# Kernel optimization log

Hardware: AMD Instinct MI355X
Metric: run time of the kernel (lower is better)

Reference implementation:

```python
import jax, jax.numpy as jnp
import numpy as np

N_NODES = 100000
N_EDGES = 3200000
NEG_SLOPE = 0.2  # PyG GATConv default
EPS = 1e-16      # PyG softmax denominator guard


def setup_inputs() -> dict:
    key = jax.random.key(0)
    ks = jax.random.split(key, 12)
    x = jax.random.normal(ks[0], (N_NODES, 4), dtype=jnp.float32)
    edge_index = jax.random.randint(ks[1], (2, N_EDGES), 0, N_NODES, dtype=jnp.int32)
    # conv1: in=4, heads=4, out=16, concat -> 64
    W1 = jax.random.normal(ks[2], (4, 64), dtype=jnp.float32) * 0.5
    a_src1 = jax.random.normal(ks[3], (4, 16), dtype=jnp.float32) * 0.3
    a_dst1 = jax.random.normal(ks[4], (4, 16), dtype=jnp.float32) * 0.3
    b1 = jnp.zeros((64,), dtype=jnp.float32)
    # conv2: in=64, heads=1, out=2, no concat
    W2 = jax.random.normal(ks[5], (64, 2), dtype=jnp.float32) * 0.2
    a_src2 = jax.random.normal(ks[6], (1, 2), dtype=jnp.float32) * 0.3
    a_dst2 = jax.random.normal(ks[7], (1, 2), dtype=jnp.float32) * 0.3
    b2 = jnp.zeros((2,), dtype=jnp.float32)
    return dict(x=x, edge_index=edge_index, W1=W1, a_src1=a_src1, a_dst1=a_dst1,
                b1=b1, W2=W2, a_src2=a_src2, a_dst2=a_dst2, b2=b2)


def _gat_layer(h_in, src, dst, W, a_s, a_d, b, heads, out_dim, concat):
    n = h_in.shape[0]
    h = (h_in @ W).reshape(n, heads, out_dim)            # [N, H, F]
    alpha_s = jnp.einsum('nhf,hf->nh', h, a_s)           # [N, H]
    alpha_d = jnp.einsum('nhf,hf->nh', h, a_d)
    e = jax.nn.leaky_relu(alpha_s[src] + alpha_d[dst], NEG_SLOPE)  # [E, H]
    # segment softmax over incoming edges of each dst node
    m = jax.ops.segment_max(e, dst, num_segments=n)      # [N, H]
    e = jnp.exp(e - m[dst])
    s = jax.ops.segment_sum(e, dst, num_segments=n)
    alpha = e / (s[dst] + EPS)                            # [E, H]
    msg = h[src] * alpha[:, :, None]                      # [E, H, F]
    out = jax.ops.segment_sum(msg, dst, num_segments=n)   # [N, H, F]
    if concat:
        out = out.reshape(n, heads * out_dim)
    else:
        out = out.mean(axis=1)
    return out + b


def reference(x, edge_index, W1, a_src1, a_dst1, b1, W2, a_src2, a_dst2, b2):
    n = x.shape[0]
    loop = jnp.arange(n, dtype=edge_index.dtype)
    src = jnp.concatenate([edge_index[0], loop])  # PyG add_self_loops=True
    dst = jnp.concatenate([edge_index[1], loop])
    h = jax.nn.elu(_gat_layer(x, src, dst, W1, a_src1, a_dst1, b1, 4, 16, True))
    h = _gat_layer(h, src, dst, W2, a_src2, a_dst2, b2, 1, 2, False)
    return jax.nn.log_softmax(h, axis=1)
```

## Files before the change

kernel.cpp:

```cpp
#include <hip/hip_runtime.h>
#include <hip/hip_fp16.h>
#include <math.h>

#define NEG_SLOPE 0.2f
#define EPS_F 1e-16f

#define P1_NB 256
#define P1S_THREADS 1024
#define MAX_BEDGES 10240

__device__ __forceinline__ float leaky(float v) {
    return v >= 0.f ? v : NEG_SLOPE * v;
}

__global__ void k_phaseA(const float* __restrict__ x, const float* __restrict__ W1,
                         const float* __restrict__ a_src1, const float* __restrict__ a_dst1,
                         __half* __restrict__ h1h, float* __restrict__ as1,
                         float* __restrict__ ad1, int N) {
    int node = blockIdx.x * 4 + (threadIdx.x >> 6);
    if (node >= N) return;
    int lane = threadIdx.x & 63;
    float x0 = x[node * 4 + 0], x1 = x[node * 4 + 1];
    float x2 = x[node * 4 + 2], x3 = x[node * 4 + 3];
    float h = x0 * W1[lane] + x1 * W1[64 + lane] + x2 * W1[128 + lane] + x3 * W1[192 + lane];
    h1h[(size_t)node * 64 + lane] = __float2half(h);
    float as = h * a_src1[lane];
    float ad = h * a_dst1[lane];
#pragma unroll
    for (int m = 8; m >= 1; m >>= 1) {
        as += __shfl_xor(as, m, 16);
        ad += __shfl_xor(ad, m, 16);
    }
    if ((lane & 15) == 0) {
        int head = lane >> 4;
        as1[node * 4 + head] = as;
        ad1[node * 4 + head] = ad;
    }
}

__global__ void k_p1hist(const int* __restrict__ dst, int* __restrict__ histT,
                         int E, int chunk, int nbucket) {
    __shared__ int cnt[512];
    int blk = blockIdx.x, t = threadIdx.x;
    for (int i = t; i < nbucket; i += P1S_THREADS) cnt[i] = 0;
    __syncthreads();
    int s = blk * chunk, e = min(E, s + chunk);
    for (int i = s + t; i < e; i += P1S_THREADS)
        atomicAdd(&cnt[dst[i] >> 8], 1);
    __syncthreads();
    for (int i = t; i < nbucket; i += P1S_THREADS)
        histT[i * P1_NB + blk] = cnt[i];
}

__global__ void k_scan1(const int* __restrict__ in, int* __restrict__ out,
                        int* __restrict__ blockSums, int M) {
    __shared__ int sdata[256];
    int t = threadIdx.x;
    int base = blockIdx.x * 2048 + t * 8;
    int v[8];
    int total = 0;
#pragma unroll
    for (int k = 0; k < 8; ++k) {
        int idx = base + k;
        v[k] = (idx < M) ? in[idx] : 0;
        total += v[k];
    }
    sdata[t] = total;
    __syncthreads();
    for (int off = 1; off < 256; off <<= 1) {
        int x = (t >= off) ? sdata[t - off] : 0;
        __syncthreads();
        sdata[t] += x;
        __syncthreads();
    }
    int run = sdata[t] - total;
#pragma unroll
    for (int k = 0; k < 8; ++k) {
        int idx = base + k;
        if (idx < M) out[idx] = run;
        run += v[k];
    }
    if (t == 255) blockSums[blockIdx.x] = sdata[255];
}

__global__ void k_scan23(int* __restrict__ out, const int* __restrict__ blockSums, int M) {
    int t = threadIdx.x;
    int base = blockIdx.x * 2048 + t * 8;
    int off = 0;
    for (int j = 0; j < (int)blockIdx.x; ++j) off += blockSums[j];
#pragma unroll
    for (int k = 0; k < 8; ++k) {
        int idx = base + k;
        if (idx < M) out[idx] += off;
    }
}

__global__ void k_p1scatter(const int* __restrict__ src, const int* __restrict__ dst,
                            const int* __restrict__ baseT, unsigned int* __restrict__ packed,
                            int E, int chunk, int nbucket) {
    __shared__ int cnt[512];
    int blk = blockIdx.x, t = threadIdx.x;
    for (int i = t; i < nbucket; i += P1S_THREADS) cnt[i] = baseT[i * P1_NB + blk];
    __syncthreads();
    int s = blk * chunk, e = min(E, s + chunk);
    for (int i = s + t; i < e; i += P1S_THREADS) {
        int d = dst[i];
        int pos = atomicAdd(&cnt[d >> 8], 1);
        packed[pos] = ((unsigned int)(d & 255) << 23) | (unsigned int)src[i];
    }
}

__global__ void k_fineL1(const unsigned int* __restrict__ packed, const int* __restrict__ baseT,
                         const __half* __restrict__ h1h, const float* __restrict__ as1,
                         const float* __restrict__ ad1, const float* __restrict__ b1,
                         const float* __restrict__ W2, const float* __restrict__ a_src2,
                         const float* __restrict__ a_dst2,
                         int* __restrict__ csr, int* __restrict__ rowptr,
                         float4* __restrict__ node2, int N, int E) {
    __shared__ int cnt[256];
    __shared__ int off[256];
    __shared__ int cur[256];
    __shared__ unsigned int eb[MAX_BEDGES];

    int b = blockIdx.x, t = threadIdx.x;
    int nbucket = gridDim.x;
    int startE = baseT[b * P1_NB];
    int endE = (b == nbucket - 1) ? E : baseT[(b + 1) * P1_NB];
    int ne = endE - startE;
    if (ne > MAX_BEDGES) ne = MAX_BEDGES;

    if (t < 256) cnt[t] = 0;
    __syncthreads();
    for (int i = t; i < ne; i += 1024)
        atomicAdd(&cnt[packed[startE + i] >> 23], 1);
    __syncthreads();
    if (t < 256) cur[t] = cnt[t];
    __syncthreads();
    for (int o = 1; o < 256; o <<= 1) {
        int v = (t < 256 && t >= o) ? cur[t - o] : 0;
        __syncthreads();
        if (t < 256) cur[t] += v;
        __syncthreads();
    }
    if (t < 256) {
        int excl = cur[t] - cnt[t];
        off[t] = excl;
        int node = (b << 8) + t;
        if (node < N) rowptr[node] = startE + excl;
    }
    if (b == 0 && t == 0) rowptr[N] = E;
    __syncthreads();
    if (t < 256) cur[t] = off[t];
    __syncthreads();
    for (int i = t; i < ne; i += 1024) {
        unsigned int p = packed[startE + i];
        int pos = atomicAdd(&cur[p >> 23], 1);
        eb[pos] = p;
    }
    __syncthreads();
    for (int i = t; i < ne; i += 1024)
        csr[startE + i] = (int)(eb[i] & 0x7FFFFFu);

    int wave = t >> 6;
    int lane = t & 63;
    int head4 = lane & 3;
    int j     = lane >> 2;
    int sub   = lane >> 4;
    int fl    = lane & 15;
    int h     = fl >> 2;
    int nodeBase = b << 8;

    for (int q = 0; q < 16; ++q) {
        int local = wave * 16 + q;
        int node = nodeBase + local;
        if (node >= N) break;
        int beg = off[local];
        int end = beg + cnt[local];

        float ad_s1 = ad1[node * 4 + head4];
        float pself4 = __expf(leaky(as1[node * 4 + head4] + ad_s1));
        float psum = (lane < 4) ? pself4 : 0.f;

        float pselfF = __shfl(pself4, h);
        float a0 = 0.f, a1 = 0.f, a2 = 0.f, a3 = 0.f;
        if (sub == 0) {
            float2 raw = *(const float2*)(h1h + ((size_t)node << 6) + (fl << 2));
            __half2 h01 = *reinterpret_cast<__half2*>(&raw.x);
            __half2 h23 = *reinterpret_cast<__half2*>(&raw.y);
            float2 f01 = __half22float2(h01), f23 = __half22float2(h23);
            a0 = pselfF * f01.x; a1 = pselfF * f01.y;
            a2 = pselfF * f23.x; a3 = pselfF * f23.y;
        }

        for (int c = beg; c < end; c += 16) {
            int e = c + j;
            bool valid = e < end;
            int s = (int)(eb[valid ? e : beg] & 0x7FFFFFu);
            float v = leaky(as1[s * 4 + head4] + ad_s1);
            float p = valid ? __expf(v) : 0.f;
            psum += p;

            int s_q[4];
#pragma unroll
            for (int m = 0; m < 4; ++m) s_q[m] = __shfl(s, m * 16 + sub * 4);
            float2 raw[4];
#pragma unroll
            for (int m = 0; m < 4; ++m)
                raw[m] = *(const float2*)(h1h + ((size_t)s_q[m] << 6) + (fl << 2));
            float p_q[4];
#pragma unroll
            for (int m = 0; m < 4; ++m) p_q[m] = __shfl(p, m * 16 + sub * 4 + h);
#pragma unroll
            for (int m = 0; m < 4; ++m) {
                __half2 h01 = *reinterpret_cast<__half2*>(&raw[m].x);
                __half2 h23 = *reinterpret_cast<__half2*>(&raw[m].y);
                float2 f01 = __half22float2(h01), f23 = __half22float2(h23);
                a0 = fmaf(p_q[m], f01.x, a0);
                a1 = fmaf(p_q[m], f01.y, a1);
                a2 = fmaf(p_q[m], f23.x, a2);
                a3 = fmaf(p_q[m], f23.y, a3);
            }
        }

        a0 += __shfl_xor(a0, 16); a0 += __shfl_xor(a0, 32);
        a1 += __shfl_xor(a1, 16); a1 += __shfl_xor(a1, 32);
        a2 += __shfl_xor(a2, 16); a2 += __shfl_xor(a2, 32);
        a3 += __shfl_xor(a3, 16); a3 += __shfl_xor(a3, 32);

#pragma unroll
        for (int m = 4; m <= 32; m <<= 1) psum += __shfl_xor(psum, m);
        float psumF = __shfl(psum, h);
        float inv = 1.f / (psumF + EPS_F);

        float4 b1v = ((const float4*)b1)[fl];
        float o0 = a0 * inv + b1v.x;
        float o1 = a1 * inv + b1v.y;
        float o2 = a2 * inv + b1v.z;
        float o3 = a3 * inv + b1v.w;
        float e0 = o0 > 0.f ? o0 : expm1f(o0);
        float e1 = o1 > 0.f ? o1 : expm1f(o1);
        float e2 = o2 > 0.f ? o2 : expm1f(o2);
        float e3 = o3 > 0.f ? o3 : expm1f(o3);

        float4 w01 = ((const float4*)W2)[fl * 2];
        float4 w23 = ((const float4*)W2)[fl * 2 + 1];
        float c0 = e0 * w01.x + e1 * w01.z + e2 * w23.x + e3 * w23.z;
        float c1 = e0 * w01.y + e1 * w01.w + e2 * w23.y + e3 * w23.w;
#pragma unroll
        for (int m = 8; m >= 1; m >>= 1) {
            c0 += __shfl_xor(c0, m);
            c1 += __shfl_xor(c1, m);
        }
        if (lane == 0) {
            float as2 = c0 * a_src2[0] + c1 * a_src2[1];
            float ad2 = c0 * a_dst2[0] + c1 * a_dst2[1];
            node2[node] = make_float4(c0, c1, as2, ad2);
        }
    }
}

__global__ void k_layer2(const int* __restrict__ rowptr, const int* __restrict__ csr,
                         const float4* __restrict__ node2, const float* __restrict__ b2,
                         float* __restrict__ out, int N) {
    int node = blockIdx.x * 16 + (threadIdx.x >> 4);
    if (node >= N) return;
    int sl = threadIdx.x & 15;

    float4 me = node2[node];
    float ad = me.w;
    int beg = rowptr[node], end = rowptr[node + 1];

    float psum = 0.f, a0 = 0.f, a1 = 0.f;
    for (int e = beg + sl; e < end; e += 16) {
        float4 sn = node2[csr[e]];
        float p = __expf(leaky(sn.z + ad));
        psum += p;
        a0 = fmaf(p, sn.x, a0);
        a1 = fmaf(p, sn.y, a1);
    }
    if (sl == 0) {
        float p = __expf(leaky(me.z + ad));
        psum += p;
        a0 = fmaf(p, me.x, a0);
        a1 = fmaf(p, me.y, a1);
    }
#pragma unroll
    for (int m = 8; m >= 1; m >>= 1) {
        psum += __shfl_xor(psum, m);
        a0 += __shfl_xor(a0, m);
        a1 += __shfl_xor(a1, m);
    }
    if (sl == 0) {
        float inv = 1.f / (psum + EPS_F);
        float o0 = a0 * inv + b2[0];
        float o1 = a1 * inv + b2[1];
        float mx = fmaxf(o0, o1);
        float lse = mx + logf(__expf(o0 - mx) + __expf(o1 - mx));
        out[node * 2 + 0] = o0 - lse;
        out[node * 2 + 1] = o1 - lse;
    }
}


extern "C" void kernel_launch(void* const* d_in, const int* in_sizes, int n_in,
                              void* d_out, int out_size, void* d_ws, size_t ws_size,
                              hipStream_t stream) {
    const float* x      = (const float*)d_in[0];
    const int*   ei     = (const int*)d_in[1];
    const float* W1     = (const float*)d_in[2];
    const float* a_src1 = (const float*)d_in[3];
    const float* a_dst1 = (const float*)d_in[4];
    const float* b1     = (const float*)d_in[5];
    const float* W2     = (const float*)d_in[6];
    const float* a_src2 = (const float*)d_in[7];
    const float* a_dst2 = (const float*)d_in[8];
    const float* b2     = (const float*)d_in[9];
    float* out = (float*)d_out;

    int N = in_sizes[0] / 4;
    int E = in_sizes[1] / 2;
    const int* e_src = ei;
    const int* e_dst = ei + E;

    int nbucket = (N + 255) >> 8;
    int M = nbucket * P1_NB;

    char* w = (char*)d_ws;
    auto alloc = [&](size_t bytes) -> void* {
        void* p = (void*)w;
        w += (bytes + 255) & ~(size_t)255;
        return p;
    };
    __half* h1h       = (__half*)alloc((size_t)N * 64 * 2);
    float*  as1       = (float*)alloc((size_t)N * 4 * 4);
    float*  ad1       = (float*)alloc((size_t)N * 4 * 4);
    float4* node2     = (float4*)alloc((size_t)N * 16);
    int*    rowptr    = (int*)alloc((size_t)(N + 1) * 4);
    int*    histT     = (int*)alloc((size_t)M * 4);
    int*    baseT     = (int*)alloc((size_t)M * 4);
    int*    blockSums = (int*)alloc(256 * 4);
    int*    csr       = (int*)alloc((size_t)E * 4);
    unsigned int* packed = (unsigned int*)alloc((size_t)E * 4);

    int chunk = (E + P1_NB - 1) / P1_NB;
    int nbScan = (M + 2047) / 2048;
    int nodeb = (N + 3) / 4;

    k_phaseA<<<nodeb, 256, 0, stream>>>(x, W1, a_src1, a_dst1, h1h, as1, ad1, N);
    k_p1hist<<<P1_NB, P1S_THREADS, 0, stream>>>(e_dst, histT, E, chunk, nbucket);
    k_scan1<<<nbScan, 256, 0, stream>>>(histT, baseT, blockSums, M);
    k_scan23<<<nbScan, 256, 0, stream>>>(baseT, blockSums, M);
    k_p1scatter<<<P1_NB, P1S_THREADS, 0, stream>>>(e_src, e_dst, baseT, packed, E, chunk, nbucket);
    k_fineL1<<<nbucket, 1024, 0, stream>>>(packed, baseT, h1h, as1, ad1, b1, W2,
                                           a_src2, a_dst2, csr, rowptr, node2, N, E);
    k_layer2<<<(N + 15) / 16, 256, 0, stream>>>(rowptr, csr, node2, b2, out, N);
}
```

Before: 249.7 us.

## Fold scan fixup into consumers, pack layer-2 node data as half, use fast ELU

Removes the k_scan23 launch by having k_p1scatter and k_fineL1 add the per-scan-block prefix computed from blockSums on the fly. Packs the layer-2 per-node record (features and attention logits) into four halves instead of four floats, halving the bytes fetched by the random gathers in k_layer2. Replaces expm1f in the ELU with __expf minus one. The half packing and fast exp lose precision, and the serial prefix loop over blockSums is done by a single thread per block.

```diff
diff --git a/kernel.cpp b/kernel.cpp
--- a/kernel.cpp
+++ b/kernel.cpp
@@ -8,6 +8,7 @@
 #define P1_NB 256
 #define P1S_THREADS 1024
 #define MAX_BEDGES 10240
+#define SCAN_SHIFT 11
 
 __device__ __forceinline__ float leaky(float v) {
     return v >= 0.f ? v : NEG_SLOPE * v;
@@ -83,24 +84,22 @@
     if (t == 255) blockSums[blockIdx.x] = sdata[255];
 }
 
-__global__ void k_scan23(int* __restrict__ out, const int* __restrict__ blockSums, int M) {
-    int t = threadIdx.x;
-    int base = blockIdx.x * 2048 + t * 8;
-    int off = 0;
-    for (int j = 0; j < (int)blockIdx.x; ++j) off += blockSums[j];
-#pragma unroll
-    for (int k = 0; k < 8; ++k) {
-        int idx = base + k;
-        if (idx < M) out[idx] += off;
-    }
-}
-
 __global__ void k_p1scatter(const int* __restrict__ src, const int* __restrict__ dst,
-                            const int* __restrict__ baseT, unsigned int* __restrict__ packed,
+                            const int* __restrict__ baseT, const int* __restrict__ blockSums,
+                            int nbScan, unsigned int* __restrict__ packed,
                             int E, int chunk, int nbucket) {
     __shared__ int cnt[512];
+    __shared__ int pre[64];
     int blk = blockIdx.x, t = threadIdx.x;
-    for (int i = t; i < nbucket; i += P1S_THREADS) cnt[i] = baseT[i * P1_NB + blk];
+    if (t == 0) {
+        int run = 0;
+        for (int j = 0; j < nbScan; ++j) { pre[j] = run; run += blockSums[j]; }
+    }
+    __syncthreads();
+    for (int i = t; i < nbucket; i += P1S_THREADS) {
+        int idx = i * P1_NB + blk;
+        cnt[i] = baseT[idx] + pre[idx >> SCAN_SHIFT];
+    }
     __syncthreads();
     int s = blk * chunk, e = min(E, s + chunk);
     for (int i = s + t; i < e; i += P1S_THREADS) {
@@ -111,26 +110,40 @@
 }
 
 __global__ void k_fineL1(const unsigned int* __restrict__ packed, const int* __restrict__ baseT,
+                         const int* __restrict__ blockSums, int nbScan,
                          const __half* __restrict__ h1h, const float* __restrict__ as1,
                          const float* __restrict__ ad1, const float* __restrict__ b1,
                          const float* __restrict__ W2, const float* __restrict__ a_src2,
                          const float* __restrict__ a_dst2,
                          int* __restrict__ csr, int* __restrict__ rowptr,
-                         float4* __restrict__ node2, int N, int E) {
+                         uint2* __restrict__ node2, int N, int E) {
     __shared__ int cnt[256];
     __shared__ int off[256];
     __shared__ int cur[256];
+    __shared__ int sePre[2];
     __shared__ unsigned int eb[MAX_BEDGES];
 
     int b = blockIdx.x, t = threadIdx.x;
     int nbucket = gridDim.x;
-    int startE = baseT[b * P1_NB];
-    int endE = (b == nbucket - 1) ? E : baseT[(b + 1) * P1_NB];
+    if (t == 0) {
+        int idx0 = b * P1_NB, idx1 = (b + 1) * P1_NB;
+        int sb0 = idx0 >> SCAN_SHIFT, sb1 = idx1 >> SCAN_SHIFT;
+        int run = 0, p0 = 0, p1 = 0;
+        for (int j = 0; j < nbScan; ++j) {
+            if (j == sb0) p0 = run;
+            if (j == sb1) p1 = run;
+            run += blockSums[j];
+        }
+        sePre[0] = p0; sePre[1] = p1;
+    }
+    if (t < 256) cnt[t] = 0;
+    __syncthreads();
+    int startE = baseT[b * P1_NB] + sePre[0];
+    int endE = E;
+    if (b != nbucket - 1) endE = baseT[(b + 1) * P1_NB] + sePre[1];
     int ne = endE - startE;
     if (ne > MAX_BEDGES) ne = MAX_BEDGES;
 
-    if (t < 256) cnt[t] = 0;
-    __syncthreads();
     for (int i = t; i < ne; i += 1024)
         atomicAdd(&cnt[packed[startE + i] >> 23], 1);
     __syncthreads();
@@ -237,10 +250,10 @@
         float o1 = a1 * inv + b1v.y;
         float o2 = a2 * inv + b1v.z;
         float o3 = a3 * inv + b1v.w;
-        float e0 = o0 > 0.f ? o0 : expm1f(o0);
-        float e1 = o1 > 0.f ? o1 : expm1f(o1);
-        float e2 = o2 > 0.f ? o2 : expm1f(o2);
-        float e3 = o3 > 0.f ? o3 : expm1f(o3);
+        float e0 = o0 > 0.f ? o0 : (__expf(o0) - 1.f);
+        float e1 = o1 > 0.f ? o1 : (__expf(o1) - 1.f);
+        float e2 = o2 > 0.f ? o2 : (__expf(o2) - 1.f);
+        float e3 = o3 > 0.f ? o3 : (__expf(o3) - 1.f);
 
         float4 w01 = ((const float4*)W2)[fl * 2];
         float4 w23 = ((const float4*)W2)[fl * 2 + 1];
@@ -254,35 +267,45 @@
         if (lane == 0) {
             float as2 = c0 * a_src2[0] + c1 * a_src2[1];
             float ad2 = c0 * a_dst2[0] + c1 * a_dst2[1];
-            node2[node] = make_float4(c0, c1, as2, ad2);
+            __half2 hc = __floats2half2_rn(c0, c1);
+            __half2 ha = __floats2half2_rn(as2, ad2);
+            node2[node] = make_uint2(*(unsigned int*)&hc, *(unsigned int*)&ha);
         }
     }
 }
 
 __global__ void k_layer2(const int* __restrict__ rowptr, const int* __restrict__ csr,
-                         const float4* __restrict__ node2, const float* __restrict__ b2,
+                         const uint2* __restrict__ node2, const float* __restrict__ b2,
                          float* __restrict__ out, int N) {
     int node = blockIdx.x * 16 + (threadIdx.x >> 4);
     if (node >= N) return;
     int sl = threadIdx.x & 15;
 
-    float4 me = node2[node];
-    float ad = me.w;
+    uint2 mraw = node2[node];
+    __half2 mch = *reinterpret_cast<__half2*>(&mraw.x);
+    __half2 mah = *reinterpret_cast<__half2*>(&mraw.y);
+    float2 mc = __half22float2(mch);
+    float2 ma = __half22float2(mah);
+    float ad = ma.y;
     int beg = rowptr[node], end = rowptr[node + 1];
 
     float psum = 0.f, a0 = 0.f, a1 = 0.f;
     for (int e = beg + sl; e < end; e += 16) {
-        float4 sn = node2[csr[e]];
-        float p = __expf(leaky(sn.z + ad));
+        uint2 sraw = node2[csr[e]];
+        __half2 sch = *reinterpret_cast<__half2*>(&sraw.x);
+        __half2 sah = *reinterpret_cast<__half2*>(&sraw.y);
+        float2 sc = __half22float2(sch);
+        float2 sa = __half22float2(sah);
+        float p = __expf(leaky(sa.x + ad));
         psum += p;
-        a0 = fmaf(p, sn.x, a0);
-        a1 = fmaf(p, sn.y, a1);
+        a0 = fmaf(p, sc.x, a0);
+        a1 = fmaf(p, sc.y, a1);
     }
     if (sl == 0) {
-        float p = __expf(leaky(me.z + ad));
+        float p = __expf(leaky(ma.x + ad));
         psum += p;
-        a0 = fmaf(p, me.x, a0);
-        a1 = fmaf(p, me.y, a1);
+        a0 = fmaf(p, mc.x, a0);
+        a1 = fmaf(p, mc.y, a1);
     }
 #pragma unroll
     for (int m = 8; m >= 1; m >>= 1) {
@@ -334,7 +357,7 @@
     __half* h1h       = (__half*)alloc((size_t)N * 64 * 2);
     float*  as1       = (float*)alloc((size_t)N * 4 * 4);
     float*  ad1       = (float*)alloc((size_t)N * 4 * 4);
-    float4* node2     = (float4*)alloc((size_t)N * 16);
+    uint2*  node2     = (uint2*)alloc((size_t)N * 8);
     int*    rowptr    = (int*)alloc((size_t)(N + 1) * 4);
     int*    histT     = (int*)alloc((size_t)M * 4);
     int*    baseT     = (int*)alloc((size_t)M * 4);
@@ -349,9 +372,10 @@
     k_phaseA<<<nodeb, 256, 0, stream>>>(x, W1, a_src1, a_dst1, h1h, as1, ad1, N);
     k_p1hist<<<P1_NB, P1S_THREADS, 0, stream>>>(e_dst, histT, E, chunk, nbucket);
     k_scan1<<<nbScan, 256, 0, stream>>>(histT, baseT, blockSums, M);
-    k_scan23<<<nbScan, 256, 0, stream>>>(baseT, blockSums, M);
-    k_p1scatter<<<P1_NB, P1S_THREADS, 0, stream>>>(e_src, e_dst, baseT, packed, E, chunk, nbucket);
-    k_fineL1<<<nbucket, 1024, 0, stream>>>(packed, baseT, h1h, as1, ad1, b1, W2,
+    k_p1scatter<<<P1_NB, P1S_THREADS, 0, stream>>>(e_src, e_dst, baseT, blockSums, nbScan,
+                                                   packed, E, chunk, nbucket);
+    k_fineL1<<<nbucket, 1024, 0, stream>>>(packed, baseT, blockSums, nbScan,
+                                           h1h, as1, ad1, b1, W2,
                                            a_src2, a_dst2, csr, rowptr, node2, N, E);
     k_layer2<<<(N + 15) / 16, 256, 0, stream>>>(rowptr, csr, node2, b2, out, N);
 }
```

Measured after the change: 244.1 us (median of 2 runs). 2.2% less time.
